# Optimization experiments

Hardware: AMD Instinct MI355X
Metric: run time of the kernel (lower is better)

The kernel has to match this reference:

```python
import jax, jax.numpy as jnp
import numpy as np

B, S, H = 2, 1024, 4096
NH, NKV, D = 32, 8, 128
EPS = 1e-6
THETA = 10000.0


def rotate_half(x):
    x1, x2 = jnp.split(x, 2, axis=-1)
    return jnp.concatenate([-x2, x1], axis=-1)


def rmsnorm(x, w, eps):
    # RMSNorm over the last (head_dim) axis
    var = jnp.mean(x * x, axis=-1, keepdims=True)
    return x * jax.lax.rsqrt(var + eps) * w


def setup_inputs() -> dict:
    key = jax.random.key(0)
    ks = jax.random.split(key, 6)
    hidden_states = jax.random.normal(ks[0], (B, S, H), dtype=jnp.float32)
    # scaled init so activations stay O(1)
    Wq = jax.random.normal(ks[1], (NH * D, H), dtype=jnp.float32) * (H ** -0.5)
    Wk = jax.random.normal(ks[2], (NKV * D, H), dtype=jnp.float32) * (H ** -0.5)
    Wv = jax.random.normal(ks[3], (NKV * D, H), dtype=jnp.float32) * (H ** -0.5)
    Wo = jax.random.normal(ks[4], (H, NH * D), dtype=jnp.float32) * ((NH * D) ** -0.5)
    q_norm_w = jnp.ones((D,), dtype=jnp.float32)
    k_norm_w = jnp.ones((D,), dtype=jnp.float32)
    # standard default RoPE cos/sin tables, broadcast to [B, S, D]
    pos = jnp.arange(S, dtype=jnp.float32)
    inv_freq = 1.0 / (THETA ** (jnp.arange(0, D, 2, dtype=jnp.float32) / D))
    freqs = pos[:, None] * inv_freq[None, :]            # [S, D/2]
    emb = jnp.concatenate([freqs, freqs], axis=-1)      # [S, D]
    cos = jnp.broadcast_to(jnp.cos(emb)[None], (B, S, D)).astype(jnp.float32)
    sin = jnp.broadcast_to(jnp.sin(emb)[None], (B, S, D)).astype(jnp.float32)
    return dict(hidden_states=hidden_states, cos=cos, sin=sin,
                Wq=Wq, Wk=Wk, Wv=Wv, Wo=Wo,
                q_norm_w=q_norm_w, k_norm_w=k_norm_w)


def reference(hidden_states, cos, sin, Wq, Wk, Wv, Wo, q_norm_w, k_norm_w):
    b, s, h = hidden_states.shape
    # fused QKV projections (MojoLinear: y = x @ W.T, no bias)
    q = (hidden_states @ Wq.T).reshape(b, s, NH, D)
    k = (hidden_states @ Wk.T).reshape(b, s, NKV, D)
    v = (hidden_states @ Wv.T).reshape(b, s, NKV, D)
    # per-head-dim RMSNorm on q and k, then [B, H, S, D] layout
    q = rmsnorm(q, q_norm_w, EPS).transpose(0, 2, 1, 3)   # [B, NH,  S, D]
    k = rmsnorm(k, k_norm_w, EPS).transpose(0, 2, 1, 3)   # [B, NKV, S, D]
    v = v.transpose(0, 2, 1, 3)                           # [B, NKV, S, D]
    # RoPE (rotate-half)
    c = cos[:, None, :, :]
    sn = sin[:, None, :, :]
    q = q * c + rotate_half(q) * sn
    k = k * c + rotate_half(k) * sn
    # GQA: expand KV heads to query heads
    groups = NH // NKV
    k = jnp.repeat(k, groups, axis=1)                     # [B, NH, S, D]
    v = jnp.repeat(v, groups, axis=1)
    # causal attention (prefill with empty paged cache == causal SDPA)
    scores = jnp.einsum('bhqd,bhkd->bhqk', q, k) * (D ** -0.5)
    causal = jnp.tril(jnp.ones((s, s), dtype=bool))
    scores = jnp.where(causal, scores, jnp.finfo(scores.dtype).min)
    probs = jax.nn.softmax(scores, axis=-1)
    out = jnp.einsum('bhqk,bhkd->bhqd', probs, v)         # [B, NH, S, D]
    out = out.transpose(0, 2, 1, 3).reshape(b, s, NH * D)
    return out @ Wo.T
```

## Files before the change

kernel.cpp:

```cpp
#include <hip/hip_runtime.h>


typedef float  f32x4   __attribute__((ext_vector_type(4)));
typedef float  f32x16  __attribute__((ext_vector_type(16)));
typedef __bf16 bf16x8  __attribute__((ext_vector_type(8)));
typedef unsigned short u16x8 __attribute__((ext_vector_type(8)));

__device__ __forceinline__ unsigned short f2b(float f) {
    union { float f; unsigned int u; } x;
    x.f = f;
    unsigned int u = x.u;
    unsigned int r = u + 0x7fffu + ((u >> 16) & 1u);
    return (unsigned short)(r >> 16);
}

__device__ __forceinline__ void async16(const unsigned short* g, unsigned short* l) {
    __builtin_amdgcn_global_load_lds(
        (const __attribute__((address_space(1))) void*)g,
        (__attribute__((address_space(3))) void*)l, 16, 0, 0);
}

__global__ __launch_bounds__(256) void cvt_all(const float* __restrict__ hsrc,
                                               const float* __restrict__ wq,
                                               const float* __restrict__ wk,
                                               const float* __restrict__ wv,
                                               const float* __restrict__ wo,
                                               unsigned short* __restrict__ hidb,
                                               unsigned short* __restrict__ wqkvb,
                                               unsigned short* __restrict__ wob) {
    int i = blockIdx.x * 256 + threadIdx.x;
    if (i >= 6291456) return;
    const float* s; unsigned short* d; int j;
    if (i < 1048576)      { s = hsrc; d = hidb;             j = i; }
    else if (i < 3145728) { s = wq;   d = wqkvb;            j = i - 1048576; }
    else if (i < 3670016) { s = wk;   d = wqkvb + 16777216; j = i - 3145728; }
    else if (i < 4194304) { s = wv;   d = wqkvb + 20971520; j = i - 3670016; }
    else                  { s = wo;   d = wob;              j = i - 4194304; }
    const float4* s4 = (const float4*)s + (size_t)j * 2;
    float4 a = s4[0], b = s4[1];
    u16x8 o;
    o[0] = f2b(a.x); o[1] = f2b(a.y); o[2] = f2b(a.z); o[3] = f2b(a.w);
    o[4] = f2b(b.x); o[5] = f2b(b.y); o[6] = f2b(b.z); o[7] = f2b(b.w);
    *((u16x8*)d + j) = o;
}

__global__ __launch_bounds__(512, 2) void gemm256_bt(const unsigned short* __restrict__ A,
                                                     const unsigned short* __restrict__ W,
                                                     float* __restrict__ C,
                                                     int K, int N) {
    __shared__ __align__(16) unsigned short Ab[3][256 * 64];
    __shared__ __align__(16) unsigned short Bb[2][192 * 64];

    const int tid  = threadIdx.x;
    const int wave = tid >> 6, lane = tid & 63;
    const int wm   = wave >> 2, wn = wave & 3;
    const int l15  = lane & 15, h = lane >> 4;
    const int cx0  = (h ^ (l15 & 7)) << 3;
    const int cx1  = cx0 ^ 32;
    const int stgrow = wave * 8 + (lane >> 3);
    const int stgcol = ((lane & 7) ^ (lane >> 3)) << 3;
    const int aRow0 = blockIdx.y * 256;
    const int bRow0 = blockIdx.x * 192;
    const int NT = K >> 6;

#define STAGE_A(t, s, bi) async16(A + (size_t)(aRow0 + (s)*64 + stgrow) * K + (t)*64 + stgcol, \
                                  &Ab[bi][(s)*4096 + wave*512])
#define STAGE_B(t, s, bi) async16(W + (size_t)(bRow0 + (s)*64 + stgrow) * K + (t)*64 + stgcol, \
                                  &Bb[bi][(s)*4096 + wave*512])
#define LOAD_AQ(q) do { \
    _Pragma("unroll") \
    for (int mi = 0; mi < 2; mi++) { \
        const unsigned short* ap = Ab_ + (wm * 128 + (q) * 32 + mi * 16 + l15) * 64; \
        af[mi][0] = *(const bf16x8*)(ap + cx0); \
        af[mi][1] = *(const bf16x8*)(ap + cx1); \
    } } while (0)
#define MFMA_Q(q) do { \
    _Pragma("unroll") \
    for (int mi = 0; mi < 2; mi++) \
    _Pragma("unroll") \
    for (int nf = 0; nf < 3; nf++) { \
        acc[(q)*2+mi][nf] = __builtin_amdgcn_mfma_f32_16x16x32_bf16(af[mi][0], bfr[nf][0], acc[(q)*2+mi][nf], 0, 0, 0); \
        acc[(q)*2+mi][nf] = __builtin_amdgcn_mfma_f32_16x16x32_bf16(af[mi][1], bfr[nf][1], acc[(q)*2+mi][nf], 0, 0, 0); \
    } } while (0)
#define SB()      __builtin_amdgcn_sched_barrier(0)
#define BARRIER() __builtin_amdgcn_s_barrier()
#define LGKM0()   asm volatile("s_waitcnt lgkmcnt(0)" ::: "memory")
#define PHASE_SYNC_IN()  do { SB(); BARRIER(); LGKM0(); SB(); } while (0)
#define PHASE_SYNC_OUT() do { SB(); BARRIER(); } while (0)

    f32x4 acc[8][3] = {};

    STAGE_B(0, 0, 0); STAGE_B(0, 1, 0); STAGE_B(0, 2, 0);
    STAGE_A(0, 0, 0); STAGE_A(0, 1, 0); STAGE_A(0, 2, 0); STAGE_A(0, 3, 0);
    STAGE_A(1, 0, 1); STAGE_A(1, 1, 1); STAGE_A(1, 2, 1); STAGE_A(1, 3, 1);
    asm volatile("s_waitcnt vmcnt(4)" ::: "memory");
    SB(); BARRIER(); SB();

    for (int t = 0; t < NT; ++t) {
        const unsigned short* Ab_ = Ab[t % 3];
        const unsigned short* Bb_ = Bb[t & 1];
        const int rb1 = (t & 1) ^ 1, ra2 = (t + 2) % 3;
        const bool sb = (t + 1 < NT), sa = (t + 2 < NT);
        bf16x8 af[2][2], bfr[3][2];

        #pragma unroll
        for (int nf = 0; nf < 3; nf++) {
            const unsigned short* bp = Bb_ + (wn * 48 + nf * 16 + l15) * 64;
            bfr[nf][0] = *(const bf16x8*)(bp + cx0);
            bfr[nf][1] = *(const bf16x8*)(bp + cx1);
        }
        LOAD_AQ(0);
        if (sb) { STAGE_B(t + 1, 0, rb1); STAGE_B(t + 1, 1, rb1); }
        PHASE_SYNC_IN();
        __builtin_amdgcn_s_setprio(1); MFMA_Q(0); __builtin_amdgcn_s_setprio(0);
        PHASE_SYNC_OUT();

        LOAD_AQ(1);
        if (sb) STAGE_B(t + 1, 2, rb1);
        if (sa) STAGE_A(t + 2, 0, ra2);
        PHASE_SYNC_IN();
        __builtin_amdgcn_s_setprio(1); MFMA_Q(1); __builtin_amdgcn_s_setprio(0);
        PHASE_SYNC_OUT();

        LOAD_AQ(2);
        if (sa) { STAGE_A(t + 2, 1, ra2); STAGE_A(t + 2, 2, ra2); }
        PHASE_SYNC_IN();
        __builtin_amdgcn_s_setprio(1); MFMA_Q(2); __builtin_amdgcn_s_setprio(0);
        PHASE_SYNC_OUT();

        LOAD_AQ(3);
        if (sa) STAGE_A(t + 2, 3, ra2);
        if (sa) asm volatile("s_waitcnt vmcnt(4)" ::: "memory");
        else    asm volatile("s_waitcnt vmcnt(0)" ::: "memory");
        PHASE_SYNC_IN();
        __builtin_amdgcn_s_setprio(1); MFMA_Q(3); __builtin_amdgcn_s_setprio(0);
        PHASE_SYNC_OUT();
    }

    #pragma unroll
    for (int mf = 0; mf < 8; mf++)
        #pragma unroll
        for (int nf = 0; nf < 3; nf++)
            #pragma unroll
            for (int r = 0; r < 4; r++) {
                int row = aRow0 + wm * 128 + mf * 16 + h * 4 + r;
                int col = bRow0 + wn * 48 + nf * 16 + l15;
                C[(size_t)row * N + col] = acc[mf][nf][r];
            }
#undef STAGE_A
#undef STAGE_B
#undef LOAD_AQ
#undef MFMA_Q
#undef SB
#undef BARRIER
#undef LGKM0
#undef PHASE_SYNC_IN
#undef PHASE_SYNC_OUT
}

__global__ __launch_bounds__(256) void gemm_bt_bf16(const unsigned short* __restrict__ A,
                                                    const unsigned short* __restrict__ W,
                                                    float* __restrict__ C,
                                                    int K, int N) {
    __shared__ __align__(16) unsigned short As[128 * 64];
    __shared__ __align__(16) unsigned short Bs[128 * 64];

    const int tid  = threadIdx.x;
    const int wave = tid >> 6, lane = tid & 63;
    const int wm   = wave >> 1, wn = wave & 1;
    const int l31  = lane & 31, lh = lane >> 5;
    const int arow = blockIdx.y * 128, brow = blockIdx.x * 128;

    int rr[4], gc[4], slot[4];
    #pragma unroll
    for (int it = 0; it < 4; it++) {
        slot[it] = it * 4 + wave;
        int ci = slot[it] * 64 + lane;
        rr[it] = ci >> 3;
        int c  = ci & 7;
        gc[it] = c ^ (rr[it] & 7);
    }

    f32x16 acc[2][2] = {};

    for (int k0 = 0; k0 < K; k0 += 64) {
        #pragma unroll
        for (int it = 0; it < 4; it++) {
            async16(A + (size_t)(arow + rr[it]) * K + k0 + gc[it] * 8, &As[slot[it] * 512]);
            async16(W + (size_t)(brow + rr[it]) * K + k0 + gc[it] * 8, &Bs[slot[it] * 512]);
        }
        __syncthreads();

        bf16x8 af[4][2], bfr[4][2];
        #pragma unroll
        for (int ks = 0; ks < 4; ks++) {
            #pragma unroll
            for (int i = 0; i < 2; i++) {
                int rowa = wm * 64 + i * 32 + l31;
                int ch   = (ks * 2 + lh) ^ (rowa & 7);
                af[ks][i]  = *(const bf16x8*)&As[rowa * 64 + ch * 8];
                int rowb = wn * 64 + i * 32 + l31;
                int chb  = (ks * 2 + lh) ^ (rowb & 7);
                bfr[ks][i] = *(const bf16x8*)&Bs[rowb * 64 + chb * 8];
            }
        }
        #pragma unroll
        for (int ks = 0; ks < 4; ks++)
            #pragma unroll
            for (int i = 0; i < 2; i++)
                #pragma unroll
                for (int j = 0; j < 2; j++)
                    acc[i][j] = __builtin_amdgcn_mfma_f32_32x32x16_bf16(af[ks][i], bfr[ks][j], acc[i][j], 0, 0, 0);
        __syncthreads();
    }

    #pragma unroll
    for (int i = 0; i < 2; i++)
        #pragma unroll
        for (int j = 0; j < 2; j++)
            #pragma unroll
            for (int r = 0; r < 16; r++) {
                int row = arow + wm * 64 + i * 32 + lh * 4 + (r & 3) + 8 * (r >> 2);
                int col = brow + wn * 64 + j * 32 + l31;
                C[(size_t)row * N + col] = acc[i][j][r];
            }
}

__global__ __launch_bounds__(256) void norm_rope(const float* __restrict__ X, int rstride,
                                                 const float* __restrict__ cosp,
                                                 const float* __restrict__ sinp,
                                                 const float* __restrict__ w,
                                                 unsigned short* __restrict__ Y, int nh) {
    const int wid  = blockIdx.x * 4 + (threadIdx.x >> 6);
    const int lane = threadIdx.x & 63;
    const int row  = wid / nh;
    const int h    = wid - row * nh;

    const float* xp = X + (size_t)row * rstride + h * 128;
    float x0 = xp[lane], x1 = xp[lane + 64];
    float ss = x0 * x0 + x1 * x1;
    #pragma unroll
    for (int off = 32; off; off >>= 1) ss += __shfl_xor(ss, off, 64);
    float r = rsqrtf(ss * (1.0f / 128.0f) + 1e-6f);
    float n0 = x0 * r * w[lane];
    float n1 = x1 * r * w[lane + 64];
    const float* cp = cosp + (size_t)row * 128;
    const float* sp = sinp + (size_t)row * 128;
    float y0 = n0 * cp[lane]      - n1 * sp[lane];
    float y1 = n1 * cp[lane + 64] + n0 * sp[lane + 64];
    const int b = row >> 10, s = row & 1023;
    unsigned short* yp = Y + (((size_t)(b * nh + h)) * 1024 + s) * 128;
    yp[lane]      = f2b(y0);
    yp[lane + 64] = f2b(y1);
}

__global__ __launch_bounds__(256) void v_trans(const float* __restrict__ V,
                                               unsigned short* __restrict__ Vt) {
    __shared__ float T[64][65];
    const int tid = threadIdx.x;
    const int st = blockIdx.x >> 1, dt = blockIdx.x & 1;
    const int bh = blockIdx.y, b = bh >> 3, h = bh & 7;

    const int sl = tid >> 2, c0 = (tid & 3) * 16;
    const float* src = V + (size_t)(b * 1024 + st * 64 + sl) * 6144 + h * 128 + dt * 64 + c0;
    #pragma unroll
    for (int j = 0; j < 4; j++) {
        float4 v = *(const float4*)(src + j * 4);
        *(float4*)&T[sl][c0 + j * 4] = v;
    }
    __syncthreads();

    const int dgrp = tid >> 6, sl2 = tid & 63;
    unsigned short* dst = Vt + (size_t)bh * 131072 + st * 64 + sl2;
    #pragma unroll
    for (int jd = 0; jd < 16; jd++) {
        int dl = dgrp * 16 + jd;
        dst[(size_t)(dt * 64 + dl) * 1024] = f2b(T[sl2][dl]);
    }
}

__global__ __launch_bounds__(256) void attn(const unsigned short* __restrict__ Qb,
                                            const unsigned short* __restrict__ Kb,
                                            const unsigned short* __restrict__ Vt,
                                            unsigned short* __restrict__ Ob) {
    __shared__ __align__(16) unsigned short Klds[128 * 128];
    __shared__ __align__(16) unsigned short Plds[4][16][136];

    const int tid  = threadIdx.x;
    const int w    = tid >> 6, lane = tid & 63;
    const int quad = lane >> 4, l15 = lane & 15;
    const int h = blockIdx.y, b = blockIdx.z, kvh = h >> 2;

    const unsigned short* Qp = Qb + ((size_t)(b * 32 + h))   * 131072;
    const unsigned short* Kp = Kb + ((size_t)(b * 8 + kvh))  * 131072;
    const unsigned short* Vp = Vt + ((size_t)(b * 8 + kvh))  * 131072;
    const float c2 = (float)(0.08838834764831845 * 1.4426950408889634);

    for (int half = 0; half < 2; half++) {
        const int qt = half ? (15 - (int)blockIdx.x) : (int)blockIdx.x;
        const int q0 = qt * 64;
        const int qrow = q0 + w * 16 + l15;

        bf16x8 qf[4];
        #pragma unroll
        for (int ks = 0; ks < 4; ks++)
            qf[ks] = *(const bf16x8*)(Qp + (size_t)qrow * 128 + ks * 32 + quad * 8);

        float m_i[4], l_i[4];
        #pragma unroll
        for (int r = 0; r < 4; r++) { m_i[r] = -1e30f; l_i[r] = 0.0f; }
        f32x4 o[8] = {};

        const int ntiles = (qt >> 1) + 1;
        const int nfull  = (qt * 64 + 1) >> 7;

        for (int kt = 0; kt < ntiles; kt++) {
            __syncthreads();
            #pragma unroll
            for (int it = 0; it < 8; it++) {
                int slot = it * 4 + w;
                int ci = slot * 64 + lane;
                int r = ci >> 4, c = ci & 15;
                int g = (c & 8) | ((c ^ r) & 7);
                async16(Kp + (size_t)(kt * 128 + r) * 128 + g * 8, &Klds[slot * 512]);
            }
            __syncthreads();

            f32x4 sacc[8] = {};
            __builtin_amdgcn_s_setprio(1);
            #pragma unroll
            for (int ks = 0; ks < 4; ks++) {
                #pragma unroll
                for (int tn = 0; tn < 8; tn++) {
                    int row = tn * 16 + l15;
                    int ch  = ks * 4 + quad;
                    int chs = (ch & 8) | ((ch ^ row) & 7);
                    bf16x8 kf = *(const bf16x8*)&Klds[row * 128 + chs * 8];
                    sacc[tn] = __builtin_amdgcn_mfma_f32_16x16x32_bf16(qf[ks], kf, sacc[tn], 0, 0, 0);
                }
            }
            __builtin_amdgcn_s_setprio(0);

            const bool masked = (kt >= nfull);
            #pragma unroll
            for (int r = 0; r < 4; r++) {
                float sv[8];
                float rmax = -1e30f;
                if (masked) {
                    const int qg = q0 + w * 16 + quad * 4 + r;
                    #pragma unroll
                    for (int tn = 0; tn < 8; tn++) {
                        float v = sacc[tn][r];
                        int kg = kt * 128 + tn * 16 + l15;
                        if (kg > qg) v = -1e30f;
                        sv[tn] = v;
                        rmax = fmaxf(rmax, v);
                    }
                } else {
                    #pragma unroll
                    for (int tn = 0; tn < 8; tn++) {
                        sv[tn] = sacc[tn][r];
                        rmax = fmaxf(rmax, sv[tn]);
                    }
                }
                #pragma unroll
                for (int off = 8; off; off >>= 1) rmax = fmaxf(rmax, __shfl_xor(rmax, off, 16));
                float mnew  = fmaxf(m_i[r], rmax);
                float alpha = __builtin_amdgcn_exp2f((m_i[r] - mnew) * c2);
                float rsum  = 0.0f;
                #pragma unroll
                for (int tn = 0; tn < 8; tn++) {
                    float p = __builtin_amdgcn_exp2f((sv[tn] - mnew) * c2);
                    sv[tn] = p;
                    rsum += p;
                }
                #pragma unroll
                for (int off = 8; off; off >>= 1) rsum += __shfl_xor(rsum, off, 16);
                m_i[r] = mnew;
                l_i[r] = l_i[r] * alpha + rsum;
                #pragma unroll
                for (int td = 0; td < 8; td++) o[td][r] *= alpha;
                #pragma unroll
                for (int tn = 0; tn < 8; tn++)
                    Plds[w][quad * 4 + r][tn * 16 + l15] = f2b(sv[tn]);
            }

            __builtin_amdgcn_s_setprio(1);
            #pragma unroll
            for (int ks = 0; ks < 4; ks++) {
                bf16x8 pf = *(const bf16x8*)&Plds[w][l15][ks * 32 + quad * 8];
                #pragma unroll
                for (int td = 0; td < 8; td++) {
                    bf16x8 vf = *(const bf16x8*)(Vp + (size_t)(td * 16 + l15) * 1024 + kt * 128 + ks * 32 + quad * 8);
                    o[td] = __builtin_amdgcn_mfma_f32_16x16x32_bf16(pf, vf, o[td], 0, 0, 0);
                }
            }
            __builtin_amdgcn_s_setprio(0);
        }

        #pragma unroll
        for (int r = 0; r < 4; r++) {
            float inv = 1.0f / l_i[r];
            const int qg = q0 + w * 16 + quad * 4 + r;
            unsigned short* op = Ob + ((size_t)(b * 1024 + qg)) * 4096 + h * 128;
            #pragma unroll
            for (int td = 0; td < 8; td++)
                op[td * 16 + l15] = f2b(o[td][r] * inv);
        }
    }
}

extern "C" void kernel_launch(void* const* d_in, const int* in_sizes, int n_in,
                              void* d_out, int out_size, void* d_ws, size_t ws_size,
                              hipStream_t stream) {
    const float* hid  = (const float*)d_in[0];
    const float* cosp = (const float*)d_in[1];
    const float* sinp = (const float*)d_in[2];
    const float* Wq   = (const float*)d_in[3];
    const float* Wk   = (const float*)d_in[4];
    const float* Wv   = (const float*)d_in[5];
    const float* Wo   = (const float*)d_in[6];
    const float* qw   = (const float*)d_in[7];
    const float* kw   = (const float*)d_in[8];
    float* out = (float*)d_out;

    char* ws = (char*)d_ws;
    float* QKVf = (float*)ws;
    unsigned short* Ob = (unsigned short*)ws;
    size_t off = (size_t)2048 * 6144 * 4;
    unsigned short* hidb  = (unsigned short*)(ws + off); off += (size_t)2048 * 4096 * 2;
    unsigned short* Wqkvb = (unsigned short*)(ws + off); off += (size_t)6144 * 4096 * 2;
    unsigned short* Wob   = (unsigned short*)(ws + off); off += (size_t)4096 * 4096 * 2;
    unsigned short* Qb    = (unsigned short*)(ws + off); off += (size_t)2048 * 4096 * 2;
    unsigned short* Kb    = (unsigned short*)(ws + off); off += (size_t)2048 * 1024 * 2;
    unsigned short* Vt    = (unsigned short*)(ws + off);

    dim3 blk(256);
    cvt_all<<<24576, blk, 0, stream>>>(hid, Wq, Wk, Wv, Wo, hidb, Wqkvb, Wob);
    gemm256_bt<<<dim3(32, 8), dim3(512), 0, stream>>>(hidb, Wqkvb, QKVf, 4096, 6144);
    norm_rope<<<16384, blk, 0, stream>>>(QKVf,        6144, cosp, sinp, qw, Qb, 32);
    norm_rope<<<4096,  blk, 0, stream>>>(QKVf + 4096, 6144, cosp, sinp, kw, Kb, 8);
    v_trans<<<dim3(32, 16), blk, 0, stream>>>(QKVf + 5120, Vt);
    attn<<<dim3(8, 32, 2), blk, 0, stream>>>(Qb, Kb, Vt, Ob);
    gemm_bt_bf16<<<dim3(32, 16), blk, 0, stream>>>(Ob, Wob, out, 4096, 4096);
}
```

Measured before the change: 518.2 us.

## Software-pipeline LDS fragment reads across phases in QKV GEMM and alias workspace

The 256x192 QKV GEMM main loop is restructured so each phase reads the next A quarter from LDS while the current quarter's MFMAs run, using partial lgkmcnt waits instead of draining to zero. The B fragments and the first A quarter for the next tile are prefetched at the end of each tile, with the loop unrolled by two to ping-pong the B register sets. Separately, the Q/K/V bf16 buffers now alias the hidden-state and weight conversion buffers to shrink the workspace. This adds register pressure, and the loop assumes an even tile count.

New measurement: 513.4 us. Within noise of the previous version (-0.9%).

```diff
diff --git a/kernel.cpp b/kernel.cpp
--- a/kernel.cpp
+++ b/kernel.cpp
@@ -67,74 +67,84 @@
                                   &Ab[bi][(s)*4096 + wave*512])
 #define STAGE_B(t, s, bi) async16(W + (size_t)(bRow0 + (s)*64 + stgrow) * K + (t)*64 + stgcol, \
                                   &Bb[bi][(s)*4096 + wave*512])
-#define LOAD_AQ(q) do { \
+#define RD_AQ(dst, buf, q) do { \
     _Pragma("unroll") \
     for (int mi = 0; mi < 2; mi++) { \
-        const unsigned short* ap = Ab_ + (wm * 128 + (q) * 32 + mi * 16 + l15) * 64; \
-        af[mi][0] = *(const bf16x8*)(ap + cx0); \
-        af[mi][1] = *(const bf16x8*)(ap + cx1); \
+        const unsigned short* ap_ = (buf) + (wm * 128 + (q) * 32 + mi * 16 + l15) * 64; \
+        dst[mi][0] = *(const bf16x8*)(ap_ + cx0); \
+        dst[mi][1] = *(const bf16x8*)(ap_ + cx1); \
     } } while (0)
-#define MFMA_Q(q) do { \
+#define RD_B(dst, buf) do { \
+    _Pragma("unroll") \
+    for (int nf = 0; nf < 3; nf++) { \
+        const unsigned short* bp_ = (buf) + (wn * 48 + nf * 16 + l15) * 64; \
+        dst[nf][0] = *(const bf16x8*)(bp_ + cx0); \
+        dst[nf][1] = *(const bf16x8*)(bp_ + cx1); \
+    } } while (0)
+#define MFMA_Q(q, AR, BR) do { \
     _Pragma("unroll") \
     for (int mi = 0; mi < 2; mi++) \
     _Pragma("unroll") \
     for (int nf = 0; nf < 3; nf++) { \
-        acc[(q)*2+mi][nf] = __builtin_amdgcn_mfma_f32_16x16x32_bf16(af[mi][0], bfr[nf][0], acc[(q)*2+mi][nf], 0, 0, 0); \
-        acc[(q)*2+mi][nf] = __builtin_amdgcn_mfma_f32_16x16x32_bf16(af[mi][1], bfr[nf][1], acc[(q)*2+mi][nf], 0, 0, 0); \
+        acc[(q)*2+mi][nf] = __builtin_amdgcn_mfma_f32_16x16x32_bf16(AR[mi][0], BR[nf][0], acc[(q)*2+mi][nf], 0, 0, 0); \
+        acc[(q)*2+mi][nf] = __builtin_amdgcn_mfma_f32_16x16x32_bf16(AR[mi][1], BR[nf][1], acc[(q)*2+mi][nf], 0, 0, 0); \
     } } while (0)
 #define SB()      __builtin_amdgcn_sched_barrier(0)
 #define BARRIER() __builtin_amdgcn_s_barrier()
-#define LGKM0()   asm volatile("s_waitcnt lgkmcnt(0)" ::: "memory")
-#define PHASE_SYNC_IN()  do { SB(); BARRIER(); LGKM0(); SB(); } while (0)
-#define PHASE_SYNC_OUT() do { SB(); BARRIER(); } while (0)
+#define PRIO1()   __builtin_amdgcn_s_setprio(1)
+#define PRIO0()   __builtin_amdgcn_s_setprio(0)
+#define LGKM(n)   asm volatile("s_waitcnt lgkmcnt(" #n ")" ::: "memory")
+
+#define TILE(T, BC, BN_) do { \
+    const int t_ = (T); \
+    const unsigned short* Ab_  = Ab[t_ % 3]; \
+    const unsigned short* AbN_ = Ab[(t_ + 1) % 3]; \
+    const unsigned short* BbN_ = Bb[(t_ + 1) & 1]; \
+    const int rb1 = (t_ & 1) ^ 1, ra2 = (t_ + 2) % 3; \
+    const bool sb = (t_ + 1 < NT), sa = (t_ + 2 < NT); \
+     \
+    RD_AQ(rB, Ab_, 1); \
+    if (sb) { STAGE_B(t_ + 1, 0, rb1); STAGE_B(t_ + 1, 1, rb1); } \
+    SB(); BARRIER(); LGKM(4); SB(); \
+    PRIO1(); MFMA_Q(0, rA, BC); PRIO0(); SB(); BARRIER(); \
+     \
+    RD_AQ(rC, Ab_, 2); \
+    if (sb) STAGE_B(t_ + 1, 2, rb1); \
+    if (sa) STAGE_A(t_ + 2, 0, ra2); \
+    SB(); BARRIER(); LGKM(4); SB(); \
+    PRIO1(); MFMA_Q(1, rB, BC); PRIO0(); SB(); BARRIER(); \
+     \
+    RD_AQ(rD, Ab_, 3); \
+    if (sa) { STAGE_A(t_ + 2, 1, ra2); STAGE_A(t_ + 2, 2, ra2); \
+              asm volatile("s_waitcnt vmcnt(3)" ::: "memory"); } \
+    else    { asm volatile("s_waitcnt vmcnt(0)" ::: "memory"); } \
+    SB(); BARRIER(); LGKM(4); SB(); \
+    PRIO1(); MFMA_Q(2, rC, BC); PRIO0(); SB(); BARRIER(); \
+     \
+    if (sb) { RD_AQ(rA, AbN_, 0); RD_B(BN_, BbN_); } \
+    if (sa) STAGE_A(t_ + 2, 3, ra2); \
+    SB(); BARRIER(); \
+    if (sb) { LGKM(10); } else { LGKM(0); } \
+    SB(); \
+    PRIO1(); MFMA_Q(3, rD, BC); PRIO0(); SB(); BARRIER(); \
+} while (0)
 
     f32x4 acc[8][3] = {};
+    bf16x8 rA[2][2], rB[2][2], rC[2][2], rD[2][2];
+    bf16x8 bc[3][2], bn[3][2];
 
     STAGE_B(0, 0, 0); STAGE_B(0, 1, 0); STAGE_B(0, 2, 0);
     STAGE_A(0, 0, 0); STAGE_A(0, 1, 0); STAGE_A(0, 2, 0); STAGE_A(0, 3, 0);
     STAGE_A(1, 0, 1); STAGE_A(1, 1, 1); STAGE_A(1, 2, 1); STAGE_A(1, 3, 1);
     asm volatile("s_waitcnt vmcnt(4)" ::: "memory");
     SB(); BARRIER(); SB();
-
-    for (int t = 0; t < NT; ++t) {
-        const unsigned short* Ab_ = Ab[t % 3];
-        const unsigned short* Bb_ = Bb[t & 1];
-        const int rb1 = (t & 1) ^ 1, ra2 = (t + 2) % 3;
-        const bool sb = (t + 1 < NT), sa = (t + 2 < NT);
-        bf16x8 af[2][2], bfr[3][2];
-
-        #pragma unroll
-        for (int nf = 0; nf < 3; nf++) {
-            const unsigned short* bp = Bb_ + (wn * 48 + nf * 16 + l15) * 64;
-            bfr[nf][0] = *(const bf16x8*)(bp + cx0);
-            bfr[nf][1] = *(const bf16x8*)(bp + cx1);
-        }
-        LOAD_AQ(0);
-        if (sb) { STAGE_B(t + 1, 0, rb1); STAGE_B(t + 1, 1, rb1); }
-        PHASE_SYNC_IN();
-        __builtin_amdgcn_s_setprio(1); MFMA_Q(0); __builtin_amdgcn_s_setprio(0);
-        PHASE_SYNC_OUT();
-
-        LOAD_AQ(1);
-        if (sb) STAGE_B(t + 1, 2, rb1);
-        if (sa) STAGE_A(t + 2, 0, ra2);
-        PHASE_SYNC_IN();
-        __builtin_amdgcn_s_setprio(1); MFMA_Q(1); __builtin_amdgcn_s_setprio(0);
-        PHASE_SYNC_OUT();
-
-        LOAD_AQ(2);
-        if (sa) { STAGE_A(t + 2, 1, ra2); STAGE_A(t + 2, 2, ra2); }
-        PHASE_SYNC_IN();
-        __builtin_amdgcn_s_setprio(1); MFMA_Q(2); __builtin_amdgcn_s_setprio(0);
-        PHASE_SYNC_OUT();
-
-        LOAD_AQ(3);
-        if (sa) STAGE_A(t + 2, 3, ra2);
-        if (sa) asm volatile("s_waitcnt vmcnt(4)" ::: "memory");
-        else    asm volatile("s_waitcnt vmcnt(0)" ::: "memory");
-        PHASE_SYNC_IN();
-        __builtin_amdgcn_s_setprio(1); MFMA_Q(3); __builtin_amdgcn_s_setprio(0);
-        PHASE_SYNC_OUT();
+    RD_B(bc, Bb[0]);
+    RD_AQ(rA, Ab[0], 0);
+    SB();
+
+    for (int t = 0; t < NT; t += 2) {
+        TILE(t,     bc, bn);
+        TILE(t + 1, bn, bc);
     }
 
     #pragma unroll
@@ -149,13 +159,15 @@
             }
 #undef STAGE_A
 #undef STAGE_B
-#undef LOAD_AQ
+#undef RD_AQ
+#undef RD_B
 #undef MFMA_Q
 #undef SB
 #undef BARRIER
-#undef LGKM0
-#undef PHASE_SYNC_IN
-#undef PHASE_SYNC_OUT
+#undef PRIO1
+#undef PRIO0
+#undef LGKM
+#undef TILE
 }
 
 __global__ __launch_bounds__(256) void gemm_bt_bf16(const unsigned short* __restrict__ A,
@@ -430,10 +442,10 @@
     size_t off = (size_t)2048 * 6144 * 4;
     unsigned short* hidb  = (unsigned short*)(ws + off); off += (size_t)2048 * 4096 * 2;
     unsigned short* Wqkvb = (unsigned short*)(ws + off); off += (size_t)6144 * 4096 * 2;
-    unsigned short* Wob   = (unsigned short*)(ws + off); off += (size_t)4096 * 4096 * 2;
-    unsigned short* Qb    = (unsigned short*)(ws + off); off += (size_t)2048 * 4096 * 2;
-    unsigned short* Kb    = (unsigned short*)(ws + off); off += (size_t)2048 * 1024 * 2;
-    unsigned short* Vt    = (unsigned short*)(ws + off);
+    unsigned short* Wob   = (unsigned short*)(ws + off);
+    unsigned short* Qb    = hidb;
+    unsigned short* Kb    = Wqkvb;
+    unsigned short* Vt    = Wqkvb + (size_t)2048 * 1024;
 
     dim3 blk(256);
     cvt_all<<<24576, blk, 0, stream>>>(hid, Wq, Wk, Wv, Wo, hidb, Wqkvb, Wob);
```
